# Optimization experiments

Hardware: AMD Instinct MI355X
Metric: run time of the kernel (lower is better)

The kernel has to match this reference:

```python
import jax, jax.numpy as jnp
import numpy as np

S = 4096          # seq_len (longformer-large-4096)
H = 1024          # hidden_size
FF = 3072         # ffnn_size (hardcoded)
G = 100           # number of gold mentions
MAX_SPAN = 30     # max_span_length
TOP_LAMBDA = 0.2
LN_EPS = 1e-5
MASK_VAL = 10000.0


def setup_inputs() -> dict:
    key = jax.random.key(0)
    ks = jax.random.split(key, 16)
    sc = 0.02
    sequence_output = jax.random.normal(ks[0], (1, S, H), jnp.float32)
    attention_mask = jnp.ones((1, S), jnp.int32)
    # valid gold spans: 1 <= start <= end < start + MAX_SPAN (so torch's >0 filter keeps all)
    gs = jax.random.randint(ks[1], (G,), 1, S - MAX_SPAN)
    gl = jax.random.randint(ks[2], (G,), 0, MAX_SPAN)
    gold_mentions = jnp.stack([gs, gs + gl], axis=1).astype(jnp.int32)  # [G, 2]
    inp = {
        'sequence_output': sequence_output,
        'attention_mask': attention_mask,
        'gold_mentions': gold_mentions,
        # start_mention_mlp
        'W_sm': jax.random.normal(ks[3], (H, FF), jnp.float32) * sc,
        'b_sm': jnp.zeros((FF,), jnp.float32),
        'g_sm': jnp.ones((FF,), jnp.float32),
        'beta_sm': jnp.zeros((FF,), jnp.float32),
        # end_mention_mlp
        'W_em': jax.random.normal(ks[4], (H, FF), jnp.float32) * sc,
        'b_em': jnp.zeros((FF,), jnp.float32),
        'g_em': jnp.ones((FF,), jnp.float32),
        'beta_em': jnp.zeros((FF,), jnp.float32),
        # classifiers
        'w_start': jax.random.normal(ks[5], (FF,), jnp.float32) * sc,
        'b_start': jnp.zeros((), jnp.float32),
        'w_end': jax.random.normal(ks[6], (FF,), jnp.float32) * sc,
        'b_end': jnp.zeros((), jnp.float32),
        'W_s2e': jax.random.normal(ks[7], (FF, FF), jnp.float32) * sc,
        'b_s2e': jnp.zeros((FF,), jnp.float32),
    }
    return inp


def _fcl(x, W, b, g, beta):
    # dense -> gelu (exact) -> layernorm (dropout is identity in eval)
    h = jax.nn.gelu(x @ W + b, approximate=False)
    mu = jnp.mean(h, axis=-1, keepdims=True)
    var = jnp.mean(jnp.square(h - mu), axis=-1, keepdims=True)
    return (h - mu) * jax.lax.rsqrt(var + LN_EPS) * g + beta


def _forward(sequence_output, attention_mask, gold_mentions,
             W_sm, b_sm, g_sm, beta_sm, W_em, b_em, g_em, beta_em,
             w_start, b_start, w_end, b_end, W_s2e, b_s2e):
    start_reps = _fcl(sequence_output, W_sm, b_sm, g_sm, beta_sm)  # [1,S,FF]
    end_reps = _fcl(sequence_output, W_em, b_em, g_em, beta_em)    # [1,S,FF]

    start_logits = jnp.einsum('bsf,f->bs', start_reps, w_start) + b_start  # [1,S]
    end_logits = jnp.einsum('bsf,f->bs', end_reps, w_end) + b_end          # [1,S]
    temp = start_reps @ W_s2e + b_s2e                                      # [1,S,FF]
    joint = jnp.einsum('bsf,btf->bst', temp, end_reps)                     # [1,S,S]
    mention_logits = joint + start_logits[:, :, None] + end_logits[:, None, :]

    # span mask: start <= end < start + MAX_SPAN (triu(0) then tril(MAX_SPAN-1))
    i = jnp.arange(S)
    mention_mask = ((i[:, None] <= i[None, :]) & (i[None, :] < i[:, None] + MAX_SPAN)
                    ).astype(jnp.float32)[None]  # [1,S,S]
    mention_logits = jnp.clip(mention_logits + (1.0 - mention_mask) * (-MASK_VAL),
                              -MASK_VAL, MASK_VAL)

    # top-k pruning; attention_mask is full so k is static: int(S * 0.2)
    max_k = int(S * TOP_LAMBDA)  # 819
    _, topk_1d = jax.lax.top_k(mention_logits.reshape(1, -1), max_k)  # [1,max_k]
    sorted_idx = jnp.sort(topk_1d, axis=-1)
    topk_start_ids = sorted_idx // S
    topk_end_ids = sorted_idx % S
    span_mask = jnp.ones((1, max_k), jnp.float32)

    # losses
    probs = jax.nn.sigmoid(mention_logits)  # [1,S,S]
    gstart = gold_mentions[:, 0]
    gend = gold_mentions[:, 1]
    gold_probs = probs[0, gstart, gend]
    # torch BCE clamps log at -100
    cost_gold = -jnp.mean(jnp.maximum(jnp.log(gold_probs), -100.0))
    junk = probs.at[0, gstart, gend].set(0.0)
    log1mp = jnp.maximum(jnp.log(1.0 - junk), -100.0)
    cost_junk = -jnp.sum(jnp.where(mention_mask == 1.0, log1mp, 0.0)) / jnp.sum(mention_mask)
    cost_is_mention = (cost_gold + cost_junk)[None]  # [1]

    return topk_start_ids, topk_end_ids, span_mask, sequence_output, cost_is_mention


def reference(sequence_output, attention_mask, gold_mentions,
              W_sm, b_sm, g_sm, beta_sm, W_em, b_em, g_em, beta_em,
              w_start, b_start, w_end, b_end, W_s2e, b_s2e):
    return _forward(sequence_output, attention_mask, gold_mentions,
                    W_sm, b_sm, g_sm, beta_sm, W_em, b_em, g_em, beta_em,
                    w_start, b_start, w_end, b_end, W_s2e, b_s2e)
```

## Files before the change

kernel.cpp:

```cpp
#include <hip/hip_runtime.h>
#include <math.h>

#define S 4096
#define H 1024
#define FF 3072
#define G 100
#define MAXSPAN 30
#define MAXK 819
#define NBAND (S * MAXSPAN)
#define BAND_COUNT 122445.0

#define O_START 0
#define O_END   819
#define O_MASK  1638
#define O_SEQ   2457
#define O_COST  (2457 + S * H)

typedef __bf16 bf16x8 __attribute__((ext_vector_type(8)));
typedef float f32x4 __attribute__((ext_vector_type(4)));


__device__ __forceinline__ float block_reduce_256(float x, volatile float* red) {
  #pragma unroll
  for (int off = 32; off > 0; off >>= 1) x += __shfl_down(x, off, 64);
  int wid = threadIdx.x >> 6;
  int lane = threadIdx.x & 63;
  __syncthreads();
  if (lane == 0) red[wid] = x;
  __syncthreads();
  return red[0] + red[1] + red[2] + red[3];
}

__device__ __forceinline__ unsigned f2key(float f) {
  unsigned b = __float_as_uint(f);
  return (b & 0x80000000u) ? ~b : (b | 0x80000000u);
}

__device__ __forceinline__ unsigned short bf16_rne(float x) {
  unsigned u = __float_as_uint(x);
  unsigned r = ((u >> 16) & 1u) + 0x7FFFu;
  return (unsigned short)((u + r) >> 16);
}

__device__ __forceinline__ void split2(float x, unsigned short& h, unsigned short& l) {
  h = bf16_rne(x);
  float hf = __uint_as_float(((unsigned)h) << 16);
  l = bf16_rne(x - hf);
}

__device__ __forceinline__ void gld16(const void* g, void* l) {
  __builtin_amdgcn_global_load_lds(
      (const __attribute__((address_space(1))) unsigned int*)g,
      (__attribute__((address_space(3))) unsigned int*)l, 16, 0, 0);
}


__global__ __launch_bounds__(256) void pack_a_kernel(const float* __restrict__ A,
                                                     unsigned short* __restrict__ hi,
                                                     unsigned short* __restrict__ lo,
                                                     int K) {
  __shared__ float tile[32][33];
  const int t = threadIdx.x;
  const int tx = t & 31, ty8 = t >> 5;
  const int k0 = blockIdx.x * 32, r0 = blockIdx.y * 32;
  #pragma unroll
  for (int r = ty8; r < 32; r += 8)
    tile[r][tx] = A[(size_t)(r0 + r) * K + k0 + tx];
  __syncthreads();
  if (t < 128) {
    const int kql = t >> 5;
    const int rl = t & 31;
    unsigned short h8[8], l8[8];
    #pragma unroll
    for (int s = 0; s < 8; s++) split2(tile[rl][kql * 8 + s], h8[s], l8[s]);
    const size_t panel = (size_t)(r0 >> 7);
    const int rloc = (r0 & 127) + rl;
    const size_t off = panel * (size_t)(128 * K) + (size_t)(k0 / 8 + kql) * 1024 + (size_t)rloc * 8;
    *(uint4*)(hi + off) = *(const uint4*)h8;
    *(uint4*)(lo + off) = *(const uint4*)l8;
  }
}

__global__ __launch_bounds__(256) void pack_bt_kernel(const float* __restrict__ W,
                                                      unsigned short* __restrict__ hi,
                                                      unsigned short* __restrict__ lo,
                                                      int K, int N) {
  __shared__ float tile[32][33];
  const int t = threadIdx.x;
  const int tx = t & 31, ty8 = t >> 5;
  const int k0 = blockIdx.x * 32, n0 = blockIdx.y * 32;
  #pragma unroll
  for (int r = ty8; r < 32; r += 8)
    tile[r][tx] = W[(size_t)(k0 + r) * N + n0 + tx];
  __syncthreads();
  if (t < 128) {
    const int kql = t >> 5;
    const int nl = t & 31;
    unsigned short h8[8], l8[8];
    #pragma unroll
    for (int s = 0; s < 8; s++) split2(tile[kql * 8 + s][nl], h8[s], l8[s]);
    const size_t panel = (size_t)(n0 >> 7);
    const int nloc = (n0 & 127) + nl;
    const size_t off = panel * (size_t)(128 * K) + (size_t)(k0 / 8 + kql) * 1024 + (size_t)nloc * 8;
    *(uint4*)(hi + off) = *(const uint4*)h8;
    *(uint4*)(lo + off) = *(const uint4*)l8;
  }
}


template <int EPI>
__global__ __launch_bounds__(256) void gemm_mfma_kernel(const unsigned short* __restrict__ Ahi,
                                                        const unsigned short* __restrict__ Alo,
                                                        const unsigned short* __restrict__ Bhi,
                                                        const unsigned short* __restrict__ Blo,
                                                        const float* __restrict__ bias,
                                                        float* __restrict__ C,
                                                        int M, int N, int K) {
  __shared__ __align__(16) char smem[32768];
  const int tid = threadIdx.x;
  const int lane = tid & 63;
  const int wid = __builtin_amdgcn_readfirstlane(tid >> 6);
  const int wm = wid >> 1, wn = wid & 1;
  const int bm = blockIdx.y * 128, bn = blockIdx.x * 128;

  const size_t panAb = (size_t)blockIdx.y * (size_t)(128 * K) * 2;
  const size_t panBb = (size_t)blockIdx.x * (size_t)(128 * K) * 2;
  const char* cAh = (const char*)Ahi + panAb;
  const char* cAl = (const char*)Alo + panAb;
  const char* cBh = (const char*)Bhi + panBb;
  const char* cBl = (const char*)Blo + panBb;
  const int lb = lane * 16;
  const int ldsq = wid * 2048;

  const int qoff = (lane >> 4) * 2048;
  const int raby = (wm * 64 + (lane & 15)) * 16;
  const int rbby = (wn * 64 + (lane & 15)) * 16;

  f32x4 acc[4][4];
  #pragma unroll
  for (int a = 0; a < 4; a++)
    #pragma unroll
    for (int b = 0; b < 4; b++) acc[a][b] = (f32x4){0.f, 0.f, 0.f, 0.f};

  for (int k0 = 0; k0 < K; k0 += 32) {
    const size_t qb = (size_t)((k0 >> 3) + wid) * 2048 + lb;
    __syncthreads();
    gld16(cAh + qb,        smem +     0 + ldsq);
    gld16(cAh + qb + 1024, smem +     0 + ldsq + 1024);
    gld16(cAl + qb,        smem +  8192 + ldsq);
    gld16(cAl + qb + 1024, smem +  8192 + ldsq + 1024);
    gld16(cBh + qb,        smem + 16384 + ldsq);
    gld16(cBh + qb + 1024, smem + 16384 + ldsq + 1024);
    gld16(cBl + qb,        smem + 24576 + ldsq);
    gld16(cBl + qb + 1024, smem + 24576 + ldsq + 1024);
    __syncthreads();

    bf16x8 ah[4], al[4], bh[4], bl[4];
    #pragma unroll
    for (int mt = 0; mt < 4; mt++) {
      ah[mt] = *(const bf16x8*)(smem +     0 + qoff + raby + mt * 256);
      al[mt] = *(const bf16x8*)(smem +  8192 + qoff + raby + mt * 256);
    }
    #pragma unroll
    for (int nt = 0; nt < 4; nt++) {
      bh[nt] = *(const bf16x8*)(smem + 16384 + qoff + rbby + nt * 256);
      bl[nt] = *(const bf16x8*)(smem + 24576 + qoff + rbby + nt * 256);
    }
    #pragma unroll
    for (int mt = 0; mt < 4; mt++)
      #pragma unroll
      for (int nt = 0; nt < 4; nt++) {
        acc[mt][nt] = __builtin_amdgcn_mfma_f32_16x16x32_bf16(ah[mt], bh[nt], acc[mt][nt], 0, 0, 0);
        acc[mt][nt] = __builtin_amdgcn_mfma_f32_16x16x32_bf16(al[mt], bh[nt], acc[mt][nt], 0, 0, 0);
        acc[mt][nt] = __builtin_amdgcn_mfma_f32_16x16x32_bf16(ah[mt], bl[nt], acc[mt][nt], 0, 0, 0);
      }
  }

  #pragma unroll
  for (int mt = 0; mt < 4; mt++) {
    #pragma unroll
    for (int nt = 0; nt < 4; nt++) {
      int row0 = bm + wm * 64 + mt * 16 + (lane >> 4) * 4;
      int col  = bn + wn * 64 + nt * 16 + (lane & 15);
      float bb = bias[col];
      #pragma unroll
      for (int r = 0; r < 4; r++) {
        float v = acc[mt][nt][r] + bb;
        if (EPI == 1) v = 0.5f * v * (1.0f + erff(v * 0.70710678118654752f));
        C[(size_t)(row0 + r) * N + col] = v;
      }
    }
  }
}


__global__ __launch_bounds__(256) void ln_dot_kernel(float* __restrict__ Hb,
                                                     const float* __restrict__ g,
                                                     const float* __restrict__ beta,
                                                     const float* __restrict__ w,
                                                     const float* __restrict__ bsc,
                                                     float* __restrict__ logits) {
  __shared__ float red[4];
  const int row = blockIdx.x, tid = threadIdx.x;
  float* h = Hb + (size_t)row * FF;

  float4 v[3];
  float s = 0.0f;
  #pragma unroll
  for (int t = 0; t < 3; t++) {
    v[t] = *(const float4*)(h + tid * 4 + t * 1024);
    s += v[t].x + v[t].y + v[t].z + v[t].w;
  }
  float mu = block_reduce_256(s, red) * (1.0f / (float)FF);

  float s2 = 0.0f;
  #pragma unroll
  for (int t = 0; t < 3; t++) {
    float dx = v[t].x - mu, dy = v[t].y - mu, dz = v[t].z - mu, dw = v[t].w - mu;
    s2 += dx * dx + dy * dy + dz * dz + dw * dw;
  }
  float var = block_reduce_256(s2, red) * (1.0f / (float)FF);
  float rstd = rsqrtf(var + 1e-5f);

  float dot = 0.0f;
  #pragma unroll
  for (int t = 0; t < 3; t++) {
    int idx = tid * 4 + t * 1024;
    float4 gv = *(const float4*)(g + idx);
    float4 bv = *(const float4*)(beta + idx);
    float4 wv = *(const float4*)(w + idx);
    float4 r;
    r.x = (v[t].x - mu) * rstd * gv.x + bv.x;
    r.y = (v[t].y - mu) * rstd * gv.y + bv.y;
    r.z = (v[t].z - mu) * rstd * gv.z + bv.z;
    r.w = (v[t].w - mu) * rstd * gv.w + bv.w;
    *(float4*)(h + idx) = r;
    dot += r.x * wv.x + r.y * wv.y + r.z * wv.z + r.w * wv.w;
  }
  float dt = block_reduce_256(dot, red);
  if (tid == 0) logits[row] = dt + bsc[0];
}


__global__ __launch_bounds__(256) void band_joint_kernel(const float* __restrict__ T,
                                                         const float* __restrict__ E,
                                                         const float* __restrict__ sl,
                                                         const float* __restrict__ el,
                                                         float* __restrict__ band) {
  __shared__ float Elds[45][260];
  const int t = threadIdx.x;
  const int i0 = blockIdx.x * 16;
  const int r_l = t >> 4, c = t & 15;

  float accd[MAXSPAN];
  #pragma unroll
  for (int d = 0; d < MAXSPAN; d++) accd[d] = 0.0f;

  for (int k0 = 0; k0 < FF; k0 += 256) {
    const float* trow = T + (size_t)(i0 + r_l) * FF + k0 + c * 16;
    float4 tv0 = *(const float4*)(trow + 0);
    float4 tv1 = *(const float4*)(trow + 4);
    float4 tv2 = *(const float4*)(trow + 8);
    float4 tv3 = *(const float4*)(trow + 12);
    __syncthreads();
    for (int rr = t >> 6; rr < 45; rr += 4) {
      int gr = i0 + rr;
      int cc = (t & 63) * 4;
      float4 ev = {0.f, 0.f, 0.f, 0.f};
      if (gr < S) ev = *(const float4*)(E + (size_t)gr * FF + k0 + cc);
      *(float4*)&Elds[rr][cc] = ev;
    }
    __syncthreads();
    #pragma unroll
    for (int d = 0; d < MAXSPAN; d++) {
      const float* er = &Elds[r_l + d][c * 16];
      float4 e0 = *(const float4*)(er + 0);
      float4 e1 = *(const float4*)(er + 4);
      float4 e2 = *(const float4*)(er + 8);
      float4 e3 = *(const float4*)(er + 12);
      accd[d] += tv0.x * e0.x + tv0.y * e0.y + tv0.z * e0.z + tv0.w * e0.w
               + tv1.x * e1.x + tv1.y * e1.y + tv1.z * e1.z + tv1.w * e1.w
               + tv2.x * e2.x + tv2.y * e2.y + tv2.z * e2.z + tv2.w * e2.w
               + tv3.x * e3.x + tv3.y * e3.y + tv3.z * e3.z + tv3.w * e3.w;
    }
  }

  const int i = i0 + r_l;
  const float my_sl = sl[i];
  #pragma unroll
  for (int d = 0; d < MAXSPAN; d++) {
    float v = accd[d];
    v += __shfl_down(v, 8, 16);
    v += __shfl_down(v, 4, 16);
    v += __shfl_down(v, 2, 16);
    v += __shfl_down(v, 1, 16);
    if (c == 0) {
      int j = i + d;
      if (j < S) {
        float vv = v + my_sl + el[j];
        vv = fminf(fmaxf(vv, -10000.0f), 10000.0f);
        band[i * MAXSPAN + d] = vv;
      } else {
        band[i * MAXSPAN + d] = -1e30f;
      }
    }
  }
}


__global__ void mark_gold_kernel(const int* __restrict__ gold, char* __restrict__ mark) {
  int t = threadIdx.x;
  if (t < G) {
    int gs = gold[2 * t], ge = gold[2 * t + 1];
    mark[gs * MAXSPAN + (ge - gs)] = 1;
  }
}

__global__ __launch_bounds__(256) void cost_junk_kernel(const float* __restrict__ band,
                                                        const char* __restrict__ mark,
                                                        double* __restrict__ jacc) {
  __shared__ float red[4];
  int e = blockIdx.x * 256 + threadIdx.x;
  int i = e / MAXSPAN, d = e - i * MAXSPAN;
  float term = 0.0f;
  if (i + d < S && !mark[e]) {
    float x = band[e];
    float p = 1.0f / (1.0f + expf(-x));
    term = fmaxf(logf(1.0f - p), -100.0f);
  }
  float ssum = block_reduce_256(term, red);
  if (threadIdx.x == 0) atomicAdd(jacc, (double)ssum);
}

__global__ __launch_bounds__(256) void finalize_kernel(const float* __restrict__ band,
                                                       const int* __restrict__ gold,
                                                       const double* __restrict__ jacc,
                                                       float* __restrict__ outc) {
  __shared__ float red[4];
  int t = threadIdx.x;
  float term = 0.0f;
  if (t < G) {
    int gs = gold[2 * t], ge = gold[2 * t + 1];
    float x = band[gs * MAXSPAN + (ge - gs)];
    float p = 1.0f / (1.0f + expf(-x));
    term = fmaxf(logf(p), -100.0f);
  }
  float sg = block_reduce_256(term, red);
  if (t == 0) {
    double cost = -((double)sg / (double)G) - ((*jacc) / BAND_COUNT);
    *outc = (float)cost;
  }
}


__global__ __launch_bounds__(1024) void topk_kernel(const float* __restrict__ band,
                                                    float* __restrict__ out) {
  __shared__ int hist[256];
  __shared__ unsigned sh_prefix;
  __shared__ int sh_remk;
  __shared__ int idxbuf[1024];
  __shared__ int tiebuf[64];
  __shared__ int cnt_gt, cnt_eq;
  __shared__ int sb[1024];
  const int tid = threadIdx.x;

  unsigned prefix = 0;
  int remk = MAXK;
  for (int pass = 0; pass < 4; pass++) {
    int shift = 24 - pass * 8;
    if (tid < 256) hist[tid] = 0;
    __syncthreads();
    for (int e = tid; e < NBAND; e += 1024) {
      unsigned key = f2key(band[e]);
      bool match = (pass == 0) || ((key >> (shift + 8)) == prefix);
      if (match) atomicAdd(&hist[(key >> shift) & 255], 1);
    }
    __syncthreads();
    if (tid == 0) {
      int cum = 0, b = 255;
      for (; b > 0; b--) {
        if (cum + hist[b] >= remk) break;
        cum += hist[b];
      }
      sh_prefix = (prefix << 8) | (unsigned)b;
      sh_remk = remk - cum;
    }
    __syncthreads();
    prefix = sh_prefix;
    remk = sh_remk;
    __syncthreads();
  }
  const unsigned T = prefix;

  if (tid == 0) { cnt_gt = 0; cnt_eq = 0; }
  __syncthreads();
  for (int e = tid; e < NBAND; e += 1024) {
    unsigned key = f2key(band[e]);
    if (key >= T) {
      int i = e / MAXSPAN, d = e - i * MAXSPAN;
      int fi = i * S + i + d;
      if (key > T) {
        int p = atomicAdd(&cnt_gt, 1);
        if (p < 1024) idxbuf[p] = fi;
      } else {
        int p = atomicAdd(&cnt_eq, 1);
        if (p < 64) tiebuf[p] = fi;
      }
    }
  }
  __syncthreads();
  if (tid == 0) {
    int ngt = cnt_gt < 1024 ? cnt_gt : 1024;
    int ne = cnt_eq < 64 ? cnt_eq : 64;
    for (int a2 = 1; a2 < ne; a2++) {
      int kv = tiebuf[a2];
      int b2 = a2 - 1;
      while (b2 >= 0 && tiebuf[b2] > kv) { tiebuf[b2 + 1] = tiebuf[b2]; b2--; }
      tiebuf[b2 + 1] = kv;
    }
    int take = remk < ne ? remk : ne;
    for (int q = 0; q < take; q++)
      if (ngt + q < 1024) idxbuf[ngt + q] = tiebuf[q];
  }
  __syncthreads();

  sb[tid] = (tid < MAXK) ? idxbuf[tid] : 0x7FFFFFFF;
  __syncthreads();
  for (int ksz = 2; ksz <= 1024; ksz <<= 1) {
    for (int jj = ksz >> 1; jj > 0; jj >>= 1) {
      int ixj = tid ^ jj;
      if (ixj > tid) {
        int a2 = sb[tid], b2 = sb[ixj];
        bool up = ((tid & ksz) == 0);
        if (up ? (a2 > b2) : (a2 < b2)) { sb[tid] = b2; sb[ixj] = a2; }
      }
      __syncthreads();
    }
  }
  if (tid < MAXK) {
    int fi = sb[tid];
    out[O_START + tid] = (float)(fi >> 12);
    out[O_END + tid]   = (float)(fi & 4095);
    out[O_MASK + tid]  = 1.0f;
  }
}


extern "C" void kernel_launch(void* const* d_in, const int* in_sizes, int n_in,
                              void* d_out, int out_size, void* d_ws, size_t ws_size,
                              hipStream_t stream) {
  (void)in_sizes; (void)n_in; (void)out_size; (void)ws_size;
  const float* seq    = (const float*)d_in[0];
  const int*   gold   = (const int*)d_in[2];
  const float* W_sm   = (const float*)d_in[3];
  const float* b_sm   = (const float*)d_in[4];
  const float* g_sm   = (const float*)d_in[5];
  const float* be_sm  = (const float*)d_in[6];
  const float* W_em   = (const float*)d_in[7];
  const float* b_em   = (const float*)d_in[8];
  const float* g_em   = (const float*)d_in[9];
  const float* be_em  = (const float*)d_in[10];
  const float* w_st   = (const float*)d_in[11];
  const float* b_st   = (const float*)d_in[12];
  const float* w_en   = (const float*)d_in[13];
  const float* b_en   = (const float*)d_in[14];
  const float* W_s2e  = (const float*)d_in[15];
  const float* b_s2e  = (const float*)d_in[16];
  float* out = (float*)d_out;
  char* ws = (char*)d_ws;

  const size_t SZ_REP = (size_t)S * FF * 4;
  float*  bufS = (float*)(ws);
  float*  bufE = (float*)(ws + SZ_REP);
  float*  bufT = (float*)(ws + 2 * SZ_REP);
  char* R3 = ws + 3 * SZ_REP;
  unsigned short* seqhi = (unsigned short*)R3;
  unsigned short* seqlo = (unsigned short*)(R3 + (size_t)S * H * 2);
  unsigned short* a3hi  = (unsigned short*)R3;
  unsigned short* a3lo  = (unsigned short*)(R3 + (size_t)S * FF * 2);
  char* R4 = ws + 4 * SZ_REP;
  unsigned short* wbhi = (unsigned short*)R4;
  unsigned short* wblo = (unsigned short*)(R4 + (size_t)FF * FF * 2);
  char* R5 = R4 + 2 * (size_t)FF * FF * 2;
  float*  band = (float*)R5;
  char*   mark = R5 + (size_t)NBAND * 4;
  double* jacc = (double*)(R5 + (size_t)NBAND * 4 + NBAND + 32);
  float*  slog = (float*)(R5 + (size_t)NBAND * 4 + NBAND + 128);
  float*  elog = slog + S;

  hipMemsetAsync(mark, 0, NBAND, stream);
  hipMemsetAsync(jacc, 0, 8, stream);

  dim3 gg(FF / 128, S / 128);

  pack_a_kernel<<<dim3(H / 32, S / 32), 256, 0, stream>>>(seq, seqhi, seqlo, H);
  pack_bt_kernel<<<dim3(H / 32, FF / 32), 256, 0, stream>>>(W_sm, wbhi, wblo, H, FF);
  gemm_mfma_kernel<1><<<gg, 256, 0, stream>>>(seqhi, seqlo, wbhi, wblo, b_sm, bufS, S, FF, H);
  ln_dot_kernel<<<S, 256, 0, stream>>>(bufS, g_sm, be_sm, w_st, b_st, slog);
  pack_bt_kernel<<<dim3(H / 32, FF / 32), 256, 0, stream>>>(W_em, wbhi, wblo, H, FF);
  gemm_mfma_kernel<1><<<gg, 256, 0, stream>>>(seqhi, seqlo, wbhi, wblo, b_em, bufE, S, FF, H);
  ln_dot_kernel<<<S, 256, 0, stream>>>(bufE, g_em, be_em, w_en, b_en, elog);
  pack_a_kernel<<<dim3(FF / 32, S / 32), 256, 0, stream>>>(bufS, a3hi, a3lo, FF);
  pack_bt_kernel<<<dim3(FF / 32, FF / 32), 256, 0, stream>>>(W_s2e, wbhi, wblo, FF, FF);
  gemm_mfma_kernel<0><<<gg, 256, 0, stream>>>(a3hi, a3lo, wbhi, wblo, b_s2e, bufT, S, FF, FF);

  band_joint_kernel<<<S / 16, 256, 0, stream>>>(bufT, bufE, slog, elog, band);

  mark_gold_kernel<<<1, 128, 0, stream>>>(gold, mark);
  cost_junk_kernel<<<NBAND / 256, 256, 0, stream>>>(band, mark, jacc);
  topk_kernel<<<1, 1024, 0, stream>>>(band, out);
  finalize_kernel<<<1, 256, 0, stream>>>(band, gold, jacc, out + O_COST);

  hipMemcpyAsync(out + O_SEQ, seq, (size_t)S * H * 4, hipMemcpyDeviceToDevice, stream);
}
```

Baseline: 888.1 us.

## Use 32x32x16 MFMA tiles and fold start LayerNorm into A packing

The GEMM inner loop switches from 16x16x32 bf16 MFMA over a 4x4 grid of accumulators to 32x32x16 MFMA over a 2x2 grid of 16-wide accumulators. The fragment addressing and the epilogue row mapping change to match. Separately, the start-branch LayerNorm no longer writes normalized values back to bufS. It stores per-row mean and rstd, and a new pack kernel applies the normalization while splitting into hi/lo bf16, saving one full write pass over the S x FF buffer. The risk is fragment-layout mismatches in the new MFMA addressing and a different LDS access pattern.

```diff
diff --git a/kernel.cpp b/kernel.cpp
--- a/kernel.cpp
+++ b/kernel.cpp
@@ -18,6 +18,7 @@
 
 typedef __bf16 bf16x8 __attribute__((ext_vector_type(8)));
 typedef float f32x4 __attribute__((ext_vector_type(4)));
+typedef float f32x16 __attribute__((ext_vector_type(16)));
 
 
 __device__ __forceinline__ float block_reduce_256(float x, volatile float* red) {
@@ -73,6 +74,47 @@
     unsigned short h8[8], l8[8];
     #pragma unroll
     for (int s = 0; s < 8; s++) split2(tile[rl][kql * 8 + s], h8[s], l8[s]);
+    const size_t panel = (size_t)(r0 >> 7);
+    const int rloc = (r0 & 127) + rl;
+    const size_t off = panel * (size_t)(128 * K) + (size_t)(k0 / 8 + kql) * 1024 + (size_t)rloc * 8;
+    *(uint4*)(hi + off) = *(const uint4*)h8;
+    *(uint4*)(lo + off) = *(const uint4*)l8;
+  }
+}
+
+__global__ __launch_bounds__(256) void pack_ln_a_kernel(const float* __restrict__ A,
+                                                        const float* __restrict__ mu,
+                                                        const float* __restrict__ rstd,
+                                                        const float* __restrict__ g,
+                                                        const float* __restrict__ beta,
+                                                        unsigned short* __restrict__ hi,
+                                                        unsigned short* __restrict__ lo,
+                                                        int K) {
+  __shared__ float tile[32][33];
+  const int t = threadIdx.x;
+  const int tx = t & 31, ty8 = t >> 5;
+  const int k0 = blockIdx.x * 32, r0 = blockIdx.y * 32;
+  #pragma unroll
+  for (int r = ty8; r < 32; r += 8)
+    tile[r][tx] = A[(size_t)(r0 + r) * K + k0 + tx];
+  __syncthreads();
+  if (t < 128) {
+    const int kql = t >> 5;
+    const int rl = t & 31;
+    const int row = r0 + rl;
+    const float m = mu[row], rs = rstd[row];
+    float4 g0 = *(const float4*)(g + k0 + kql * 8);
+    float4 g1 = *(const float4*)(g + k0 + kql * 8 + 4);
+    float4 b0 = *(const float4*)(beta + k0 + kql * 8);
+    float4 b1 = *(const float4*)(beta + k0 + kql * 8 + 4);
+    float gv[8] = {g0.x, g0.y, g0.z, g0.w, g1.x, g1.y, g1.z, g1.w};
+    float bv[8] = {b0.x, b0.y, b0.z, b0.w, b1.x, b1.y, b1.z, b1.w};
+    unsigned short h8[8], l8[8];
+    #pragma unroll
+    for (int s = 0; s < 8; s++) {
+      float v = (tile[rl][kql * 8 + s] - m) * rs * gv[s] + bv[s];
+      split2(v, h8[s], l8[s]);
+    }
     const size_t panel = (size_t)(r0 >> 7);
     const int rloc = (r0 & 127) + rl;
     const size_t off = panel * (size_t)(128 * K) + (size_t)(k0 / 8 + kql) * 1024 + (size_t)rloc * 8;
@@ -132,15 +174,18 @@
   const int lb = lane * 16;
   const int ldsq = wid * 2048;
 
-  const int qoff = (lane >> 4) * 2048;
-  const int raby = (wm * 64 + (lane & 15)) * 16;
-  const int rbby = (wn * 64 + (lane & 15)) * 16;
-
-  f32x4 acc[4][4];
-  #pragma unroll
-  for (int a = 0; a < 4; a++)
-    #pragma unroll
-    for (int b = 0; b < 4; b++) acc[a][b] = (f32x4){0.f, 0.f, 0.f, 0.f};
+  const int khalf = lane >> 5;
+  const int r31 = lane & 31;
+  const int abase = khalf * 2048 + (wm * 64 + r31) * 16;
+  const int bbase = khalf * 2048 + (wn * 64 + r31) * 16;
+
+  f32x16 acc[2][2];
+  #pragma unroll
+  for (int a = 0; a < 2; a++)
+    #pragma unroll
+    for (int b = 0; b < 2; b++)
+      #pragma unroll
+      for (int r = 0; r < 16; r++) acc[a][b][r] = 0.0f;
 
   for (int k0 = 0; k0 < K; k0 += 32) {
     const size_t qb = (size_t)((k0 >> 3) + wid) * 2048 + lb;
@@ -155,51 +200,60 @@
     gld16(cBl + qb + 1024, smem + 24576 + ldsq + 1024);
     __syncthreads();
 
-    bf16x8 ah[4], al[4], bh[4], bl[4];
-    #pragma unroll
-    for (int mt = 0; mt < 4; mt++) {
-      ah[mt] = *(const bf16x8*)(smem +     0 + qoff + raby + mt * 256);
-      al[mt] = *(const bf16x8*)(smem +  8192 + qoff + raby + mt * 256);
-    }
-    #pragma unroll
-    for (int nt = 0; nt < 4; nt++) {
-      bh[nt] = *(const bf16x8*)(smem + 16384 + qoff + rbby + nt * 256);
-      bl[nt] = *(const bf16x8*)(smem + 24576 + qoff + rbby + nt * 256);
-    }
-    #pragma unroll
-    for (int mt = 0; mt < 4; mt++)
+    bf16x8 ah[2][2], al[2][2], bh[2][2], bl[2][2];
+    #pragma unroll
+    for (int ks = 0; ks < 2; ks++) {
       #pragma unroll
-      for (int nt = 0; nt < 4; nt++) {
-        acc[mt][nt] = __builtin_amdgcn_mfma_f32_16x16x32_bf16(ah[mt], bh[nt], acc[mt][nt], 0, 0, 0);
-        acc[mt][nt] = __builtin_amdgcn_mfma_f32_16x16x32_bf16(al[mt], bh[nt], acc[mt][nt], 0, 0, 0);
-        acc[mt][nt] = __builtin_amdgcn_mfma_f32_16x16x32_bf16(ah[mt], bl[nt], acc[mt][nt], 0, 0, 0);
-      }
-  }
-
-  #pragma unroll
-  for (int mt = 0; mt < 4; mt++) {
-    #pragma unroll
-    for (int nt = 0; nt < 4; nt++) {
-      int row0 = bm + wm * 64 + mt * 16 + (lane >> 4) * 4;
-      int col  = bn + wn * 64 + nt * 16 + (lane & 15);
-      float bb = bias[col];
+      for (int mt = 0; mt < 2; mt++) {
+        ah[ks][mt] = *(const bf16x8*)(smem +     0 + ks * 4096 + abase + mt * 512);
+        al[ks][mt] = *(const bf16x8*)(smem +  8192 + ks * 4096 + abase + mt * 512);
+      }
       #pragma unroll
-      for (int r = 0; r < 4; r++) {
-        float v = acc[mt][nt][r] + bb;
+      for (int nt = 0; nt < 2; nt++) {
+        bh[ks][nt] = *(const bf16x8*)(smem + 16384 + ks * 4096 + bbase + nt * 512);
+        bl[ks][nt] = *(const bf16x8*)(smem + 24576 + ks * 4096 + bbase + nt * 512);
+      }
+    }
+    #pragma unroll
+    for (int ks = 0; ks < 2; ks++)
+      #pragma unroll
+      for (int mt = 0; mt < 2; mt++)
+        #pragma unroll
+        for (int nt = 0; nt < 2; nt++) {
+          acc[mt][nt] = __builtin_amdgcn_mfma_f32_32x32x16_bf16(ah[ks][mt], bh[ks][nt], acc[mt][nt], 0, 0, 0);
+          acc[mt][nt] = __builtin_amdgcn_mfma_f32_32x32x16_bf16(al[ks][mt], bh[ks][nt], acc[mt][nt], 0, 0, 0);
+          acc[mt][nt] = __builtin_amdgcn_mfma_f32_32x32x16_bf16(ah[ks][mt], bl[ks][nt], acc[mt][nt], 0, 0, 0);
+        }
+  }
+
+  #pragma unroll
+  for (int mt = 0; mt < 2; mt++) {
+    #pragma unroll
+    for (int nt = 0; nt < 2; nt++) {
+      const int colg = bn + wn * 64 + nt * 32 + r31;
+      const float bb = bias[colg];
+      #pragma unroll
+      for (int reg = 0; reg < 16; reg++) {
+        const int rowl = (reg & 3) + 8 * (reg >> 2) + 4 * khalf;
+        const int rowg = bm + wm * 64 + mt * 32 + rowl;
+        float v = acc[mt][nt][reg] + bb;
         if (EPI == 1) v = 0.5f * v * (1.0f + erff(v * 0.70710678118654752f));
-        C[(size_t)(row0 + r) * N + col] = v;
-      }
-    }
-  }
-}
-
-
+        C[(size_t)rowg * N + colg] = v;
+      }
+    }
+  }
+}
+
+
+template <int WRITEBACK>
 __global__ __launch_bounds__(256) void ln_dot_kernel(float* __restrict__ Hb,
                                                      const float* __restrict__ g,
                                                      const float* __restrict__ beta,
                                                      const float* __restrict__ w,
                                                      const float* __restrict__ bsc,
-                                                     float* __restrict__ logits) {
+                                                     float* __restrict__ logits,
+                                                     float* __restrict__ mu_out,
+                                                     float* __restrict__ rstd_out) {
   __shared__ float red[4];
   const int row = blockIdx.x, tid = threadIdx.x;
   float* h = Hb + (size_t)row * FF;
@@ -234,11 +288,14 @@
     r.y = (v[t].y - mu) * rstd * gv.y + bv.y;
     r.z = (v[t].z - mu) * rstd * gv.z + bv.z;
     r.w = (v[t].w - mu) * rstd * gv.w + bv.w;
-    *(float4*)(h + idx) = r;
+    if (WRITEBACK) *(float4*)(h + idx) = r;
     dot += r.x * wv.x + r.y * wv.y + r.z * wv.z + r.w * wv.w;
   }
   float dt = block_reduce_256(dot, red);
-  if (tid == 0) logits[row] = dt + bsc[0];
+  if (tid == 0) {
+    logits[row] = dt + bsc[0];
+    if (!WRITEBACK) { mu_out[row] = mu; rstd_out[row] = rstd; }
+  }
 }
 
 
@@ -487,6 +544,8 @@
   double* jacc = (double*)(R5 + (size_t)NBAND * 4 + NBAND + 32);
   float*  slog = (float*)(R5 + (size_t)NBAND * 4 + NBAND + 128);
   float*  elog = slog + S;
+  float*  muS  = elog + S;
+  float*  rstdS = muS + S;
 
   hipMemsetAsync(mark, 0, NBAND, stream);
   hipMemsetAsync(jacc, 0, 8, stream);
@@ -496,11 +555,11 @@
   pack_a_kernel<<<dim3(H / 32, S / 32), 256, 0, stream>>>(seq, seqhi, seqlo, H);
   pack_bt_kernel<<<dim3(H / 32, FF / 32), 256, 0, stream>>>(W_sm, wbhi, wblo, H, FF);
   gemm_mfma_kernel<1><<<gg, 256, 0, stream>>>(seqhi, seqlo, wbhi, wblo, b_sm, bufS, S, FF, H);
-  ln_dot_kernel<<<S, 256, 0, stream>>>(bufS, g_sm, be_sm, w_st, b_st, slog);
+  ln_dot_kernel<0><<<S, 256, 0, stream>>>(bufS, g_sm, be_sm, w_st, b_st, slog, muS, rstdS);
   pack_bt_kernel<<<dim3(H / 32, FF / 32), 256, 0, stream>>>(W_em, wbhi, wblo, H, FF);
   gemm_mfma_kernel<1><<<gg, 256, 0, stream>>>(seqhi, seqlo, wbhi, wblo, b_em, bufE, S, FF, H);
-  ln_dot_kernel<<<S, 256, 0, stream>>>(bufE, g_em, be_em, w_en, b_en, elog);
-  pack_a_kernel<<<dim3(FF / 32, S / 32), 256, 0, stream>>>(bufS, a3hi, a3lo, FF);
+  ln_dot_kernel<1><<<S, 256, 0, stream>>>(bufE, g_em, be_em, w_en, b_en, elog, nullptr, nullptr);
+  pack_ln_a_kernel<<<dim3(FF / 32, S / 32), 256, 0, stream>>>(bufS, muS, rstdS, g_sm, be_sm, a3hi, a3lo, FF);
   pack_bt_kernel<<<dim3(FF / 32, FF / 32), 256, 0, stream>>>(W_s2e, wbhi, wblo, FF, FF);
   gemm_mfma_kernel<0><<<gg, 256, 0, stream>>>(a3hi, a3lo, wbhi, wblo, b_s2e, bufT, S, FF, FF);
 
```

New measurement: 839.4 us. -5.5%, faster.
